# Kernel optimization log

Hardware: AMD Instinct MI355X
Metric: run time of the kernel (lower is better)

The kernel has to match this reference:

```python
import jax, jax.numpy as jnp
import numpy as np

H = 8            # num_heads
DK = 256         # head_qk_dim
DV = 512         # head_v_dim
EPS = 1e-5
ROPE_BASE = 10000.0


def _rope(x):
    # x: [B, T, H, DK]; GPT-NeoX style (non-interleaved halves), seqlen_offset=0
    B, T, h, d = x.shape
    inv_freq = 1.0 / (ROPE_BASE ** (jnp.arange(0, d, 2, dtype=jnp.float32) / d))  # [d/2]
    t = jnp.arange(T, dtype=jnp.float32)
    freqs = t[:, None] * inv_freq[None, :]              # [T, d/2]
    cos = jnp.cos(freqs)[None, :, None, :]              # [1, T, 1, d/2]
    sin = jnp.sin(freqs)[None, :, None, :]
    x1, x2 = x[..., : d // 2], x[..., d // 2 :]
    return jnp.concatenate([x1 * cos - x2 * sin, x2 * cos + x1 * sin], axis=-1)


def setup_inputs() -> dict:
    key = jax.random.key(0)
    ks = jax.random.split(key, 7)
    hidden = 2048
    B, T = 2, 2048
    w = 0.02
    return {
        "hidden_states": jax.random.normal(ks[0], (B, T, hidden), jnp.float32),
        "Wq": jax.random.normal(ks[1], (hidden, H * DK), jnp.float32) * w,
        "Wk": jax.random.normal(ks[2], (hidden, H * DK), jnp.float32) * w,
        "Wv": jax.random.normal(ks[3], (hidden, H * DV), jnp.float32) * w,
        "Wg": jax.random.normal(ks[4], (hidden, H * DV), jnp.float32) * w,
        "Wo": jax.random.normal(ks[5], (H * DV, hidden), jnp.float32) * w,
        "g_norm_weight": jnp.ones((DV,), jnp.float32),
    }


def reference(hidden_states, Wq, Wk, Wv, Wg, Wo, g_norm_weight):
    B, T, _ = hidden_states.shape
    q = (hidden_states @ Wq).reshape(B, T, H, DK)
    k = (hidden_states @ Wk).reshape(B, T, H, DK)
    v = (hidden_states @ Wv).reshape(B, T, H, DV)
    g = (hidden_states @ Wg).reshape(B, T, H, DV)

    q = _rope(q)
    k = _rope(k)

    # per-head RetNet decay: gamma_h = 1 - 2^(-5-h)
    gamma = 1.0 - jnp.exp2(-5.0 - jnp.arange(H, dtype=jnp.float32))     # [H]
    idx = jnp.arange(T)
    diff = idx[:, None] - idx[None, :]                                   # [T, T]
    causal = diff >= 0
    log2g = jnp.log2(gamma)[:, None, None]                               # [H,1,1]
    D = jnp.where(causal[None], jnp.exp2(log2g * jnp.where(causal, diff, 0)[None]), 0.0)  # [H,T,T]

    scale = DK ** -0.5
    scores = jnp.einsum("bihd,bjhd->bhij", q * scale, k) * D[None]       # [B,H,T,T]
    o = jnp.einsum("bhij,bjhd->bihd", scores, v)                          # [B,T,H,DV]

    # fused RMSNorm (per head over DV) + swish gate
    rms = jax.lax.rsqrt(jnp.mean(o * o, axis=-1, keepdims=True) + EPS)
    o = o * rms * g_norm_weight
    o = o * (g * jax.nn.sigmoid(g))

    return o.reshape(B, T, H * DV) @ Wo
```

## Files before the change

kernel.cpp:

```cpp
#include <hip/hip_runtime.h>
#include <hip/hip_bf16.h>
#include <math.h>

#define NH 8
#define DKk 256
#define DVv 512
#define Bn 2
#define Tn 2048
#define HID 2048
#define EPSf 1e-5f

typedef __bf16 bf16x8 __attribute__((ext_vector_type(8)));
typedef float f32x4 __attribute__((ext_vector_type(4)));
typedef unsigned short us8 __attribute__((ext_vector_type(8)));
using bf16 = __hip_bfloat16;
typedef unsigned short ushort_t;

__device__ __forceinline__ void gload_lds16(const void* g, void* lds_base) {
  __builtin_amdgcn_global_load_lds(
      (const __attribute__((address_space(1))) void*)g,
      (__attribute__((address_space(3))) void*)lds_base, 16, 0, 0);
}

__device__ __forceinline__ ushort_t f2bf_raw(float f) {
  bf16 h = __float2bfloat16(f);
  return *reinterpret_cast<ushort_t*>(&h);
}
__device__ __forceinline__ float bf2f_raw(ushort_t u) {
  union { unsigned int i; float f; } v; v.i = ((unsigned int)u) << 16; return v.f;
}

__global__ void k_f32_to_bf16(const float4* __restrict__ in, ushort4* __restrict__ out, int n4) {
  int i = blockIdx.x * blockDim.x + threadIdx.x;
  if (i >= n4) return;
  float4 v = in[i];
  ushort4 o;
  o.x = f2bf_raw(v.x); o.y = f2bf_raw(v.y); o.z = f2bf_raw(v.z); o.w = f2bf_raw(v.w);
  out[i] = o;
}

__global__ void k_transpose_w(const float* __restrict__ W, bf16* __restrict__ WT, int K, int N) {
  __shared__ float t[32][33];
  int n0 = blockIdx.x * 32, k0 = blockIdx.y * 32;
  int tx = threadIdx.x, ty = threadIdx.y;
#pragma unroll
  for (int i = 0; i < 4; i++)
    t[ty + i * 8][tx] = W[(size_t)(k0 + ty + i * 8) * N + n0 + tx];
  __syncthreads();
#pragma unroll
  for (int i = 0; i < 4; i++)
    WT[(size_t)(n0 + ty + i * 8) * K + k0 + tx] = __float2bfloat16(t[tx][ty + i * 8]);
}

__global__ void k_build_vS(const ushort_t* __restrict__ v, ushort_t* __restrict__ vS) {
  __shared__ ushort_t t[32 * 520];
  const int tid = threadIdx.x;
  const int kt = blockIdx.x;
  const int bh = blockIdx.y;
  const int b = bh >> 3, h = bh & 7;
#pragma unroll
  for (int r = 0; r < 8; r++) {
    int j = r * 4 + (tid >> 6);
    int vec = tid & 63;
    us8 d = *(const us8*)(v + (((size_t)(b * Tn + kt * 32 + j) * NH + h) * DVv) + vec * 8);
    *(us8*)(&t[j * 520 + vec * 8]) = d;
  }
  __syncthreads();
#pragma unroll
  for (int u = 0; u < 8; u++) {
    int uid = u * 256 + tid;
    int chunk = uid >> 9;
    int dv = uid & 511;
    us8 o;
#pragma unroll
    for (int jj = 0; jj < 8; jj++) o[jj] = t[(chunk * 8 + jj) * 520 + dv];
    *(us8*)(vS + ((size_t)(bh * 64 + kt) * 2048 + chunk * 512 + dv) * 8) = o;
  }
}

__global__ void k_rope(bf16* __restrict__ x, float scale) {
  int tid = blockIdx.x * 256 + threadIdx.x;
  int i = tid & 127;
  int h = (tid >> 7) & 7;
  int t = (tid >> 10) & (Tn - 1);
  int b = tid >> 21;
  float inv = exp2f(-(float)i * (13.287712379549449f / 128.0f));
  float ang = (float)t * inv;
  float s, c;
  sincosf(ang, &s, &c);
  size_t base = ((size_t)(b * Tn + t) * NH + h) * DKk + i;
  float x1 = __bfloat162float(x[base]);
  float x2 = __bfloat162float(x[base + 128]);
  x[base]       = __float2bfloat16((x1 * c - x2 * s) * scale);
  x[base + 128] = __float2bfloat16((x2 * c + x1 * s) * scale);
}

template <bool OUT_BF16>
__global__ __launch_bounds__(256) void k_gemm(const bf16* __restrict__ A, const bf16* __restrict__ BT,
                                              void* __restrict__ Cout, int M, int N, int K) {
  __shared__ __align__(16) bf16 a_lds[128 * 32];
  __shared__ __align__(16) bf16 b_lds[128 * 32];
  const int tid = threadIdx.x;
  const int l = tid & 63;
  const int w = tid >> 6;
  const int wr = w >> 1, wc = w & 1;
  const int m0 = blockIdx.y * 128, n0 = blockIdx.x * 128;
  const int quad = l >> 4, c16 = l & 15;

  const int lrow = l >> 2;
  const int loff = (l & 3) * 16;
  const char* aG0 = (const char*)(A + (size_t)(m0 + w * 32 + lrow) * K) + loff;
  const char* aG1 = (const char*)(A + (size_t)(m0 + w * 32 + 16 + lrow) * K) + loff;
  const char* bG0 = (const char*)(BT + (size_t)(n0 + w * 32 + lrow) * K) + loff;
  const char* bG1 = (const char*)(BT + (size_t)(n0 + w * 32 + 16 + lrow) * K) + loff;
  char* aL0 = (char*)a_lds + w * 2048;
  char* aL1 = (char*)a_lds + w * 2048 + 1024;
  char* bL0 = (char*)b_lds + w * 2048;
  char* bL1 = (char*)b_lds + w * 2048 + 1024;

  f32x4 acc[4][4];
  const f32x4 fz = {0.f, 0.f, 0.f, 0.f};
#pragma unroll
  for (int r = 0; r < 4; r++)
#pragma unroll
    for (int c = 0; c < 4; c++) acc[r][c] = fz;

  for (int k0 = 0; k0 < K; k0 += 32) {
    __syncthreads();
    size_t kb = (size_t)k0 * 2;
    gload_lds16(aG0 + kb, aL0);
    gload_lds16(aG1 + kb, aL1);
    gload_lds16(bG0 + kb, bL0);
    gload_lds16(bG1 + kb, bL1);
    __syncthreads();
    bf16x8 af[4], bfv[4];
#pragma unroll
    for (int r = 0; r < 4; r++)
      af[r] = *(const bf16x8*)(a_lds + (wr * 64 + r * 16 + c16) * 32 + quad * 8);
#pragma unroll
    for (int c = 0; c < 4; c++)
      bfv[c] = *(const bf16x8*)(b_lds + (wc * 64 + c * 16 + c16) * 32 + quad * 8);
#pragma unroll
    for (int r = 0; r < 4; r++)
#pragma unroll
      for (int c = 0; c < 4; c++)
        acc[r][c] = __builtin_amdgcn_mfma_f32_16x16x32_bf16(af[r], bfv[c], acc[r][c], 0, 0, 0);
  }

#pragma unroll
  for (int r = 0; r < 4; r++)
#pragma unroll
    for (int c = 0; c < 4; c++)
#pragma unroll
      for (int rr = 0; rr < 4; rr++) {
        int m = m0 + wr * 64 + r * 16 + quad * 4 + rr;
        int n = n0 + wc * 64 + c * 16 + c16;
        float val = acc[r][c][rr];
        if (OUT_BF16) ((bf16*)Cout)[(size_t)m * N + n] = __float2bfloat16(val);
        else          ((float*)Cout)[(size_t)m * N + n] = val;
      }
}

#define BARX() asm volatile("s_barrier" ::: "memory")
#define LGKM0() { asm volatile("s_waitcnt lgkmcnt(0)" ::: "memory"); __builtin_amdgcn_sched_barrier(0); }
#define VMW4() asm volatile("s_waitcnt vmcnt(4)" ::: "memory")
#define VMW0() asm volatile("s_waitcnt vmcnt(0)" ::: "memory")
#define PRIO1 __builtin_amdgcn_s_setprio(1)
#define PRIO0 __builtin_amdgcn_s_setprio(0)

#define QUADX(MH, NH)                                                              \
  { _Pragma("unroll") for (int kk_ = 0; kk_ < 2; ++kk_)                            \
    _Pragma("unroll") for (int mf_ = 0; mf_ < 4; ++mf_)                            \
    _Pragma("unroll") for (int nf_ = 0; nf_ < 2; ++nf_)                            \
      acc[(MH)*4 + mf_][(NH)*2 + nf_] = __builtin_amdgcn_mfma_f32_16x16x32_bf16(   \
          ar[(MH)*4 + mf_][kk_], br[(NH)*2 + nf_][kk_],                            \
          acc[(MH)*4 + mf_][(NH)*2 + nf_], 0, 0, 0); }

__global__ __launch_bounds__(512, 2) void k_gemm8(const bf16* __restrict__ A, const bf16* __restrict__ BT,
                                                  bf16* __restrict__ O0, bf16* __restrict__ O1,
                                                  int nsplit, int M, int Ntot, int K) {
  extern __shared__ char lds[];
  const int tid = threadIdx.x;
  const int lane = tid & 63;
  const int w = tid >> 6;
  const int wr = w >> 2;
  const int wc = w & 3;
  const int quad = lane >> 4, c16 = lane & 15;
  const int m0 = blockIdx.y * 256, n0 = blockIdx.x * 256;

  const int srow = (w << 4) | (lane >> 3);
  const int gsw = (((lane & 7) ^ (lane >> 3)) << 4);
  const size_t rowBytes = (size_t)K * 2;
  const char* aS = (const char*)(A + (size_t)(m0 + srow) * K) + gsw;
  const char* bS = (const char*)(BT + (size_t)(n0 + srow) * K) + gsw;

  auto stage = [&](int matB, int buf, int h, int t) {
    const char* base = (matB ? bS : aS) + (size_t)h * 128 * rowBytes + (size_t)t * 128;
    char* ldst = lds + buf * 65536 + matB * 32768 + h * 16384 + w * 2048;
    gload_lds16(base, ldst);
    gload_lds16(base + 8 * rowBytes, ldst + 1024);
  };
  auto ldA = [&](int buf, int mf, int kk) -> bf16x8 {
    int row = wr * 128 + mf * 16 + c16;
    return *(const bf16x8*)(lds + buf * 65536 + row * 128 + ((((kk << 2) | quad) ^ (c16 & 7)) << 4));
  };
  auto ldB = [&](int buf, int nf, int kk) -> bf16x8 {
    int row = wc * 64 + nf * 16 + c16;
    return *(const bf16x8*)(lds + buf * 65536 + 32768 + row * 128 + ((((kk << 2) | quad) ^ (c16 & 7)) << 4));
  };

  f32x4 acc[8][4];
  const f32x4 fz = {0.f, 0.f, 0.f, 0.f};
#pragma unroll
  for (int i = 0; i < 8; i++)
#pragma unroll
    for (int j = 0; j < 4; j++) acc[i][j] = fz;
  bf16x8 ar[8][2], br[4][2];

  const int nT = K >> 6;
  const int nIter = nT >> 1;

  stage(0, 0, 0, 0); stage(0, 0, 1, 0);
  stage(1, 0, 0, 0); stage(1, 0, 1, 0);
  stage(0, 1, 0, 1); stage(0, 1, 1, 1);
  VMW4();
  BARX();

  for (int it = 0; it < nIter; ++it) {
    const int t = it * 2;
    const bool last = (it == nIter - 1);
#pragma unroll
    for (int mf = 0; mf < 4; ++mf) { ar[mf][0] = ldA(0, mf, 0); ar[mf][1] = ldA(0, mf, 1); }
#pragma unroll
    for (int nf = 0; nf < 2; ++nf) { br[nf][0] = ldB(0, nf, 0); br[nf][1] = ldB(0, nf, 1); }
    stage(1, 1, 0, t + 1);
    BARX(); LGKM0();
    PRIO1; QUADX(0, 0); PRIO0;
    BARX();
#pragma unroll
    for (int mf = 4; mf < 8; ++mf) { ar[mf][0] = ldA(0, mf, 0); ar[mf][1] = ldA(0, mf, 1); }
#pragma unroll
    for (int nf = 2; nf < 4; ++nf) { br[nf][0] = ldB(0, nf, 0); br[nf][1] = ldB(0, nf, 1); }
    stage(1, 1, 1, t + 1);
    BARX(); LGKM0();
    PRIO1; QUADX(0, 1); PRIO0;
    BARX();
    if (!last) stage(0, 0, 0, t + 2);
    BARX();
    PRIO1; QUADX(1, 0); PRIO0;
    BARX();
    if (!last) stage(0, 0, 1, t + 2);
    BARX();
    PRIO1; QUADX(1, 1); PRIO0;
    if (!last) { VMW4(); } else { VMW0(); }
    BARX();
#pragma unroll
    for (int mf = 0; mf < 4; ++mf) { ar[mf][0] = ldA(1, mf, 0); ar[mf][1] = ldA(1, mf, 1); }
#pragma unroll
    for (int nf = 0; nf < 2; ++nf) { br[nf][0] = ldB(1, nf, 0); br[nf][1] = ldB(1, nf, 1); }
    if (!last) stage(1, 0, 0, t + 2);
    BARX(); LGKM0();
    PRIO1; QUADX(0, 0); PRIO0;
    BARX();
#pragma unroll
    for (int mf = 4; mf < 8; ++mf) { ar[mf][0] = ldA(1, mf, 0); ar[mf][1] = ldA(1, mf, 1); }
#pragma unroll
    for (int nf = 2; nf < 4; ++nf) { br[nf][0] = ldB(1, nf, 0); br[nf][1] = ldB(1, nf, 1); }
    if (!last) stage(1, 0, 1, t + 2);
    BARX(); LGKM0();
    PRIO1; QUADX(0, 1); PRIO0;
    BARX();
    if (!last) stage(0, 1, 0, t + 3);
    BARX();
    PRIO1; QUADX(1, 0); PRIO0;
    BARX();
    if (!last) stage(0, 1, 1, t + 3);
    BARX();
    PRIO1; QUADX(1, 1); PRIO0;
    if (!last) VMW4();
    BARX();
  }

  bf16* Ob; int ldo, nc0;
  if (n0 < nsplit) { Ob = O0; ldo = nsplit; nc0 = n0; }
  else             { Ob = O1; ldo = Ntot - nsplit; nc0 = n0 - nsplit; }
#pragma unroll
  for (int mf = 0; mf < 8; ++mf)
#pragma unroll
    for (int nf = 0; nf < 4; ++nf)
#pragma unroll
      for (int rr = 0; rr < 4; ++rr) {
        int m = m0 + wr * 128 + mf * 16 + quad * 4 + rr;
        int n = nc0 + wc * 64 + nf * 16 + c16;
        Ob[(size_t)m * ldo + n] = __float2bfloat16(acc[mf][nf][rr]);
      }
}

__global__ __launch_bounds__(256, 2) void k_retention(const bf16* __restrict__ q, const bf16* __restrict__ k,
                                                      const char* __restrict__ vS, const bf16* __restrict__ g,
                                                      const float* __restrict__ gnw, bf16* __restrict__ X) {
  __shared__ __align__(16) char smem[65536];
  bf16* k_lds = (bf16*)smem;
  char* v_lds = smem + 16384;
  ushort_t* p_lds = (ushort_t*)(smem + 49152);
  float* red = (float*)(smem + 54272);
  bf16* o_lds = (bf16*)smem;

  const int tid = threadIdx.x;
  const int l = tid & 63, w = tid >> 6;
  const int quad = l >> 4, c16 = l & 15;

  const int bid = blockIdx.x;
  const int xcd = bid & 7;
  const int slot = bid >> 3;
  const int bh = xcd + 8 * (slot & 1);
  const int b = bh >> 3, h = bh & 7;
  const int qt = 31 - (slot >> 1);
  const int q0 = qt * 64;

  bf16x8 qf[8];
  {
    const bf16* qrow = q + ((size_t)(b * Tn + q0 + w * 16 + c16) * NH + h) * DKk + quad * 8;
#pragma unroll
    for (int c = 0; c < 8; c++) qf[c] = *(const bf16x8*)(qrow + c * 32);
  }

  const float log2g = log2f(1.0f - exp2f(-5.0f - (float)h));

  f32x4 acc[4][8];
  const f32x4 fz = {0.f, 0.f, 0.f, 0.f};
#pragma unroll
  for (int rt = 0; rt < 4; rt++)
#pragma unroll
    for (int n = 0; n < 8; n++) acc[rt][n] = fz;

  const int ktmax = 2 * qt + 1;
  const float Dcut = 30.0f / (-log2g);
  int kt0 = (int)fmaxf(0.0f, floorf(((float)q0 - Dcut) * (1.0f / 32.0f)));

  const char* vS_tilebase = vS + (size_t)(bh * 64) * 32768;

  for (int kt = kt0; kt <= ktmax; kt++) {
    __syncthreads();
#pragma unroll
    for (int i = 0; i < 4; i++) {
      int instr = w * 4 + i;
      int j = instr * 2 + (l >> 5);
      int chunk_g = (l & 31) ^ (j & 7);
      const char* gp = (const char*)(k + ((size_t)(b * Tn + kt * 32 + j) * NH + h) * DKk) + chunk_g * 16;
      gload_lds16(gp, (char*)k_lds + instr * 1024);
    }
#pragma unroll
    for (int i = 0; i < 8; i++) {
      int instr = w * 8 + i;
      const char* gp = vS_tilebase + (size_t)kt * 32768 + instr * 1024 + l * 16;
      gload_lds16(gp, v_lds + instr * 1024);
    }
    __syncthreads();

    f32x4 sacc[2] = {fz, fz};
#pragma unroll
    for (int jt = 0; jt < 2; jt++)
#pragma unroll
      for (int c = 0; c < 8; c++) {
        const char* kp = (const char*)k_lds + (jt * 16 + c16) * 512 + (((c * 4 + quad) ^ (c16 & 7)) * 16);
        bf16x8 bfrag = *(const bf16x8*)kp;
        sacc[jt] = __builtin_amdgcn_mfma_f32_16x16x32_bf16(qf[c], bfrag, sacc[jt], 0, 0, 0);
      }

#pragma unroll
    for (int jt = 0; jt < 2; jt++)
#pragma unroll
      for (int r = 0; r < 4; r++) {
        int ig = q0 + w * 16 + quad * 4 + r;
        int jg = kt * 32 + jt * 16 + c16;
        int d = ig - jg;
        float val = (d >= 0) ? sacc[jt][r] * exp2f(log2g * (float)d) : 0.0f;
        p_lds[(w * 16 + quad * 4 + r) * 40 + jt * 16 + c16] = f2bf_raw(val);
      }
    __syncthreads();

    bf16x8 pa[4];
#pragma unroll
    for (int rt = 0; rt < 4; rt++)
      pa[rt] = *(const bf16x8*)((const char*)p_lds + (rt * 16 + c16) * 80 + quad * 16);
#pragma unroll
    for (int n = 0; n < 8; n++) {
      bf16x8 bv = *(const bf16x8*)(v_lds + quad * 8192 + (w * 128 + n * 16 + c16) * 16);
#pragma unroll
      for (int rt = 0; rt < 4; rt++)
        acc[rt][n] = __builtin_amdgcn_mfma_f32_16x16x32_bf16(pa[rt], bv, acc[rt][n], 0, 0, 0);
    }
  }

  __syncthreads();
#pragma unroll
  for (int rt = 0; rt < 4; rt++)
#pragma unroll
    for (int r = 0; r < 4; r++) {
      float s = 0.f;
#pragma unroll
      for (int n = 0; n < 8; n++) { float v = acc[rt][n][r]; s += v * v; }
      s += __shfl_xor(s, 1);
      s += __shfl_xor(s, 2);
      s += __shfl_xor(s, 4);
      s += __shfl_xor(s, 8);
      if (c16 == 0) red[(rt * 16 + quad * 4 + r) * 4 + w] = s;
    }
  __syncthreads();
  float ss[4][4];
#pragma unroll
  for (int rt = 0; rt < 4; rt++)
#pragma unroll
    for (int r = 0; r < 4; r++) {
      int row = rt * 16 + quad * 4 + r;
      float tot = red[row * 4] + red[row * 4 + 1] + red[row * 4 + 2] + red[row * 4 + 3];
      ss[rt][r] = rsqrtf(tot * (1.0f / DVv) + EPSf);
    }
  __syncthreads();

#pragma unroll
  for (int n = 0; n < 8; n++) {
    int col = w * 128 + n * 16 + c16;
    float gw = gnw[col];
#pragma unroll
    for (int rt = 0; rt < 4; rt++)
#pragma unroll
      for (int r = 0; r < 4; r++) {
        int row = rt * 16 + quad * 4 + r;
        o_lds[row * 512 + col] = __float2bfloat16(acc[rt][n][r] * ss[rt][r] * gw);
      }
  }
  __syncthreads();

#pragma unroll
  for (int it = 0; it < 16; it++) {
    int cid = it * 256 + tid;
    int row = cid >> 6;
    int cp = (cid & 63) * 8;
    const ushort_t* gp = (const ushort_t*)g + ((size_t)(b * Tn + q0 + row) * NH + h) * DVv + cp;
    us8 gv = *(const us8*)gp;
    us8 ov;
#pragma unroll
    for (int e = 0; e < 8; e++) {
      float gf = bf2f_raw(gv[e]);
      float gate = gf / (1.0f + expf(-gf));
      float of = __bfloat162float(o_lds[row * 512 + cp + e]);
      ov[e] = f2bf_raw(of * gate);
    }
    *(us8*)((ushort_t*)X + ((size_t)(b * Tn + q0 + row) * NH + h) * DVv + cp) = ov;
  }
}

extern "C" void kernel_launch(void* const* d_in, const int* in_sizes, int n_in,
                              void* d_out, int out_size, void* d_ws, size_t ws_size,
                              hipStream_t stream) {
  const float* hs  = (const float*)d_in[0];
  const float* Wq  = (const float*)d_in[1];
  const float* Wk  = (const float*)d_in[2];
  const float* Wv  = (const float*)d_in[3];
  const float* Wg  = (const float*)d_in[4];
  const float* Wo  = (const float*)d_in[5];
  const float* gnw = (const float*)d_in[6];
  float* out = (float*)d_out;
  char* ws = (char*)d_ws;

  bf16* hsb = (bf16*)(ws);
  bf16* WqT = (bf16*)(ws + 16777216);
  bf16* WkT = (bf16*)(ws + 25165824);
  bf16* WvT = (bf16*)(ws + 33554432);
  bf16* WgT = (bf16*)(ws + 50331648);
  char* vSb = ws;
  bf16* WoT = (bf16*)(ws + 33554432);
  bf16* qb = (bf16*)(ws + 67108864);
  bf16* kb = (bf16*)(ws + 83886080);
  bf16* vb = (bf16*)(ws + 100663296);
  bf16* gb = (bf16*)(ws + 134217728);
  bf16* Xb = vb;

  static bool attr_done = false;
  if (!attr_done) {
    hipFuncSetAttribute((const void*)k_gemm8, hipFuncAttributeMaxDynamicSharedMemorySize, 131072);
    attr_done = true;
  }

  dim3 tb(32, 8);

  k_f32_to_bf16<<<8192, 256, 0, stream>>>((const float4*)hs, (ushort4*)hsb, 2097152);
  k_transpose_w<<<dim3(HID / 32, HID / 32), tb, 0, stream>>>(Wq, WqT, HID, HID);
  k_transpose_w<<<dim3(HID / 32, HID / 32), tb, 0, stream>>>(Wk, WkT, HID, HID);
  k_transpose_w<<<dim3(NH * DVv / 32, HID / 32), tb, 0, stream>>>(Wv, WvT, HID, NH * DVv);
  k_transpose_w<<<dim3(NH * DVv / 32, HID / 32), tb, 0, stream>>>(Wg, WgT, HID, NH * DVv);
  k_gemm8<<<dim3(16, 16), 512, 131072, stream>>>(hsb, WqT, qb, kb, 2048, 4096, 4096, 2048);
  k_gemm8<<<dim3(32, 16), 512, 131072, stream>>>(hsb, WvT, vb, gb, 4096, 4096, 8192, 2048);
  k_rope<<<16384, 256, 0, stream>>>(qb, 0.0625f);
  k_rope<<<16384, 256, 0, stream>>>(kb, 1.0f);
  k_build_vS<<<dim3(64, 16), 256, 0, stream>>>((const ushort_t*)vb, (ushort_t*)vSb);
  k_transpose_w<<<dim3(HID / 32, NH * DVv / 32), tb, 0, stream>>>(Wo, WoT, NH * DVv, HID);
  k_retention<<<512, 256, 0, stream>>>(qb, kb, vSb, gb, gnw, Xb);
  k_gemm<false><<<dim3(16, 32), 256, 0, stream>>>(Xb, WoT, out, 4096, 2048, 4096);
}
```

Baseline: 684.4 us.

## Swizzle GEMM block order across XCDs, deepen prefetch, double-buffer K and stream V directly

New measurement: 695.2 us. No clear change (+1.6%).

```diff
diff --git a/kernel.cpp b/kernel.cpp
--- a/kernel.cpp
+++ b/kernel.cpp
@@ -104,7 +104,11 @@
   const int l = tid & 63;
   const int w = tid >> 6;
   const int wr = w >> 1, wc = w & 1;
-  const int m0 = blockIdx.y * 128, n0 = blockIdx.x * 128;
+  const int bid = blockIdx.y * gridDim.x + blockIdx.x;
+  const int cpx = (gridDim.x * gridDim.y) >> 3;
+  const int s = (bid & 7) * cpx + (bid >> 3);
+  const int bx = s / gridDim.y, by = s % gridDim.y;
+  const int m0 = by * 128, n0 = bx * 128;
   const int quad = l >> 4, c16 = l & 15;
 
   const int lrow = l >> 2;
@@ -163,18 +167,18 @@
 
 #define BARX() asm volatile("s_barrier" ::: "memory")
 #define LGKM0() { asm volatile("s_waitcnt lgkmcnt(0)" ::: "memory"); __builtin_amdgcn_sched_barrier(0); }
-#define VMW4() asm volatile("s_waitcnt vmcnt(4)" ::: "memory")
+#define VMW8() asm volatile("s_waitcnt vmcnt(8)" ::: "memory")
 #define VMW0() asm volatile("s_waitcnt vmcnt(0)" ::: "memory")
 #define PRIO1 __builtin_amdgcn_s_setprio(1)
 #define PRIO0 __builtin_amdgcn_s_setprio(0)
 
-#define QUADX(MH, NH)                                                              \
+#define QUADX(MH, NHh)                                                             \
   { _Pragma("unroll") for (int kk_ = 0; kk_ < 2; ++kk_)                            \
     _Pragma("unroll") for (int mf_ = 0; mf_ < 4; ++mf_)                            \
     _Pragma("unroll") for (int nf_ = 0; nf_ < 2; ++nf_)                            \
-      acc[(MH)*4 + mf_][(NH)*2 + nf_] = __builtin_amdgcn_mfma_f32_16x16x32_bf16(   \
-          ar[(MH)*4 + mf_][kk_], br[(NH)*2 + nf_][kk_],                            \
-          acc[(MH)*4 + mf_][(NH)*2 + nf_], 0, 0, 0); }
+      acc[(MH)*4 + mf_][(NHh)*2 + nf_] = __builtin_amdgcn_mfma_f32_16x16x32_bf16(  \
+          ar[(MH)*4 + mf_][kk_], br[(NHh)*2 + nf_][kk_],                           \
+          acc[(MH)*4 + mf_][(NHh)*2 + nf_], 0, 0, 0); }
 
 __global__ __launch_bounds__(512, 2) void k_gemm8(const bf16* __restrict__ A, const bf16* __restrict__ BT,
                                                   bf16* __restrict__ O0, bf16* __restrict__ O1,
@@ -186,7 +190,11 @@
   const int wr = w >> 2;
   const int wc = w & 3;
   const int quad = lane >> 4, c16 = lane & 15;
-  const int m0 = blockIdx.y * 256, n0 = blockIdx.x * 256;
+  const int bid = blockIdx.y * gridDim.x + blockIdx.x;
+  const int cpx = (gridDim.x * gridDim.y) >> 3;
+  const int sw = (bid & 7) * cpx + (bid >> 3);
+  const int bx = sw / gridDim.y, by = sw % gridDim.y;
+  const int m0 = by * 256, n0 = bx * 256;
 
   const int srow = (w << 4) | (lane >> 3);
   const int gsw = (((lane & 7) ^ (lane >> 3)) << 4);
@@ -223,7 +231,8 @@
   stage(0, 0, 0, 0); stage(0, 0, 1, 0);
   stage(1, 0, 0, 0); stage(1, 0, 1, 0);
   stage(0, 1, 0, 1); stage(0, 1, 1, 1);
-  VMW4();
+  stage(1, 1, 0, 1); stage(1, 1, 1, 1);
+  VMW8();
   BARX();
 
   for (int it = 0; it < nIter; ++it) {
@@ -233,7 +242,6 @@
     for (int mf = 0; mf < 4; ++mf) { ar[mf][0] = ldA(0, mf, 0); ar[mf][1] = ldA(0, mf, 1); }
 #pragma unroll
     for (int nf = 0; nf < 2; ++nf) { br[nf][0] = ldB(0, nf, 0); br[nf][1] = ldB(0, nf, 1); }
-    stage(1, 1, 0, t + 1);
     BARX(); LGKM0();
     PRIO1; QUADX(0, 0); PRIO0;
     BARX();
@@ -241,24 +249,22 @@
     for (int mf = 4; mf < 8; ++mf) { ar[mf][0] = ldA(0, mf, 0); ar[mf][1] = ldA(0, mf, 1); }
 #pragma unroll
     for (int nf = 2; nf < 4; ++nf) { br[nf][0] = ldB(0, nf, 0); br[nf][1] = ldB(0, nf, 1); }
-    stage(1, 1, 1, t + 1);
     BARX(); LGKM0();
     PRIO1; QUADX(0, 1); PRIO0;
     BARX();
-    if (!last) stage(0, 0, 0, t + 2);
+    if (!last) { stage(0, 0, 0, t + 2); stage(0, 0, 1, t + 2); }
     BARX();
     PRIO1; QUADX(1, 0); PRIO0;
     BARX();
-    if (!last) stage(0, 0, 1, t + 2);
+    if (!last) { stage(1, 0, 0, t + 2); stage(1, 0, 1, t + 2); }
     BARX();
     PRIO1; QUADX(1, 1); PRIO0;
-    if (!last) { VMW4(); } else { VMW0(); }
+    if (!last) { VMW8(); } else { VMW0(); }
     BARX();
 #pragma unroll
     for (int mf = 0; mf < 4; ++mf) { ar[mf][0] = ldA(1, mf, 0); ar[mf][1] = ldA(1, mf, 1); }
 #pragma unroll
     for (int nf = 0; nf < 2; ++nf) { br[nf][0] = ldB(1, nf, 0); br[nf][1] = ldB(1, nf, 1); }
-    if (!last) stage(1, 0, 0, t + 2);
     BARX(); LGKM0();
     PRIO1; QUADX(0, 0); PRIO0;
     BARX();
@@ -266,18 +272,17 @@
     for (int mf = 4; mf < 8; ++mf) { ar[mf][0] = ldA(1, mf, 0); ar[mf][1] = ldA(1, mf, 1); }
 #pragma unroll
     for (int nf = 2; nf < 4; ++nf) { br[nf][0] = ldB(1, nf, 0); br[nf][1] = ldB(1, nf, 1); }
-    if (!last) stage(1, 0, 1, t + 2);
     BARX(); LGKM0();
     PRIO1; QUADX(0, 1); PRIO0;
     BARX();
-    if (!last) stage(0, 1, 0, t + 3);
+    if (!last) { stage(0, 1, 0, t + 3); stage(0, 1, 1, t + 3); }
     BARX();
     PRIO1; QUADX(1, 0); PRIO0;
     BARX();
-    if (!last) stage(0, 1, 1, t + 3);
+    if (!last) { stage(1, 1, 0, t + 3); stage(1, 1, 1, t + 3); }
     BARX();
     PRIO1; QUADX(1, 1); PRIO0;
-    if (!last) VMW4();
+    if (!last) VMW8();
     BARX();
   }
 
@@ -300,10 +305,8 @@
                                                       const char* __restrict__ vS, const bf16* __restrict__ g,
                                                       const float* __restrict__ gnw, bf16* __restrict__ X) {
   __shared__ __align__(16) char smem[65536];
-  bf16* k_lds = (bf16*)smem;
-  char* v_lds = smem + 16384;
-  ushort_t* p_lds = (ushort_t*)(smem + 49152);
-  float* red = (float*)(smem + 54272);
+  ushort_t* p_lds = (ushort_t*)(smem + 32768);
+  float* red = (float*)(smem + 38912);
   bf16* o_lds = (bf16*)smem;
 
   const int tid = threadIdx.x;
@@ -340,30 +343,30 @@
 
   const char* vS_tilebase = vS + (size_t)(bh * 64) * 32768;
 
-  for (int kt = kt0; kt <= ktmax; kt++) {
-    __syncthreads();
+  auto stageK = [&](int kt, int pbuf) {
 #pragma unroll
     for (int i = 0; i < 4; i++) {
       int instr = w * 4 + i;
       int j = instr * 2 + (l >> 5);
       int chunk_g = (l & 31) ^ (j & 7);
       const char* gp = (const char*)(k + ((size_t)(b * Tn + kt * 32 + j) * NH + h) * DKk) + chunk_g * 16;
-      gload_lds16(gp, (char*)k_lds + instr * 1024);
+      gload_lds16(gp, smem + pbuf * 16384 + instr * 1024);
     }
-#pragma unroll
-    for (int i = 0; i < 8; i++) {
-      int instr = w * 8 + i;
-      const char* gp = vS_tilebase + (size_t)kt * 32768 + instr * 1024 + l * 16;
-      gload_lds16(gp, v_lds + instr * 1024);
-    }
+  };
+
+  stageK(kt0, 0);
+
+  for (int kt = kt0; kt <= ktmax; kt++) {
+    const int pb = (kt - kt0) & 1;
     __syncthreads();
+    if (kt < ktmax) stageK(kt + 1, pb ^ 1);
 
     f32x4 sacc[2] = {fz, fz};
 #pragma unroll
     for (int jt = 0; jt < 2; jt++)
 #pragma unroll
       for (int c = 0; c < 8; c++) {
-        const char* kp = (const char*)k_lds + (jt * 16 + c16) * 512 + (((c * 4 + quad) ^ (c16 & 7)) * 16);
+        const char* kp = smem + pb * 16384 + (jt * 16 + c16) * 512 + (((c * 4 + quad) ^ (c16 & 7)) * 16);
         bf16x8 bfrag = *(const bf16x8*)kp;
         sacc[jt] = __builtin_amdgcn_mfma_f32_16x16x32_bf16(qf[c], bfrag, sacc[jt], 0, 0, 0);
       }
@@ -378,15 +381,18 @@
         float val = (d >= 0) ? sacc[jt][r] * exp2f(log2g * (float)d) : 0.0f;
         p_lds[(w * 16 + quad * 4 + r) * 40 + jt * 16 + c16] = f2bf_raw(val);
       }
-    __syncthreads();
+    asm volatile("s_waitcnt lgkmcnt(0)" ::: "memory");
+    __builtin_amdgcn_sched_barrier(0);
+    __builtin_amdgcn_s_barrier();
 
     bf16x8 pa[4];
 #pragma unroll
     for (int rt = 0; rt < 4; rt++)
       pa[rt] = *(const bf16x8*)((const char*)p_lds + (rt * 16 + c16) * 80 + quad * 16);
+    const char* vt = vS_tilebase + (size_t)kt * 32768 + quad * 8192 + w * 2048 + c16 * 16;
 #pragma unroll
     for (int n = 0; n < 8; n++) {
-      bf16x8 bv = *(const bf16x8*)(v_lds + quad * 8192 + (w * 128 + n * 16 + c16) * 16);
+      bf16x8 bv = *(const bf16x8*)(vt + n * 256);
 #pragma unroll
       for (int rt = 0; rt < 4; rt++)
         acc[rt][n] = __builtin_amdgcn_mfma_f32_16x16x32_bf16(pa[rt], bv, acc[rt][n], 0, 0, 0);
```
